# Performance work log

Measured on AMD Instinct MI355X. Metric: run time of the kernel, lower is better.

## Reference

```python
import jax, jax.numpy as jnp
import numpy as np


def _ln(x, w, b):
    m = jnp.mean(x, axis=-1, keepdims=True)
    v = jnp.var(x, axis=-1, keepdims=True)
    return (x - m) / jnp.sqrt(v + 1e-5) * w + b


def setup_inputs() -> dict:
    B, T, C = 4, 2048, 1024
    E_RWKV, E = 2, 3          # 2 RWKV experts + 1 transformer expert
    H = 4 * C                 # RWKV FFN hidden
    S = 0.02                  # init scale
    key = jax.random.key(0)
    ks = jax.random.split(key, 20)
    d = {}
    d["x"] = jax.random.normal(ks[0], (B, T, C), jnp.float32)
    d["v_first"] = jax.random.normal(ks[1], (B, T, C), jnp.float32)
    d["capital_shares"] = jax.random.uniform(ks[2], (E,), jnp.float32)
    # layer norms
    d["ln1_w"] = jnp.ones((C,), jnp.float32)
    d["ln1_b"] = jnp.zeros((C,), jnp.float32)
    d["ln2_w"] = jnp.ones((C,), jnp.float32)
    d["ln2_b"] = jnp.zeros((C,), jnp.float32)
    # simplified RWKV time-mix (gated linear attention stand-in)
    d["Wr"] = S * jax.random.normal(ks[3], (C, C), jnp.float32)
    d["Wv"] = S * jax.random.normal(ks[4], (C, C), jnp.float32)
    d["Wo"] = S * jax.random.normal(ks[5], (C, C), jnp.float32)
    d["Ws"] = S * jax.random.normal(ks[6], (C, C), jnp.float32)
    # RWKV FFN experts (squared-ReLU channel mix)
    d["K_rwkv"] = S * jax.random.normal(ks[7], (E_RWKV, C, H), jnp.float32)
    d["V_rwkv"] = S * jax.random.normal(ks[8], (E_RWKV, H, C), jnp.float32)
    d["conf_rwkv"] = S * jax.random.normal(ks[9], (E_RWKV, C), jnp.float32)
    # transformer expert (state-gated)
    d["W1"] = S * jax.random.normal(ks[10], (C, C), jnp.float32)
    d["W2"] = S * jax.random.normal(ks[11], (C, C), jnp.float32)
    d["W3"] = S * jax.random.normal(ks[12], (C, C), jnp.float32)
    d["conf_trans"] = S * jax.random.normal(ks[13], (C,), jnp.float32)
    # critic
    d["w_diff"] = S * jax.random.normal(ks[14], (C,), jnp.float32)
    d["W_aff"] = S * jax.random.normal(ks[15], (C, E), jnp.float32)
    # bridge (h -> rwkv_state reconstruction)
    d["W_bridge"] = S * jax.random.normal(ks[16], (C, C), jnp.float32)
    return d


def reference(x, v_first, capital_shares, ln1_w, ln1_b, ln2_w, ln2_b,
              Wr, Wv, Wo, Ws, K_rwkv, V_rwkv, conf_rwkv,
              W1, W2, W3, conf_trans, w_diff, W_aff, W_bridge):
    B, T, C = x.shape
    # attention (simplified time-mix): gated linear projection + state head
    xln = _ln(x, ln1_w, ln1_b)
    att_out = (jax.nn.sigmoid(xln @ Wr) * (xln @ Wv)) @ Wo
    rwkv_state = xln @ Ws
    x = x + att_out
    h = _ln(x, ln2_w, ln2_b)

    # per-expert confidences  (B, T, E)
    conf_r = jax.nn.sigmoid(jnp.einsum('btc,ec->bte', h, conf_rwkv))
    conf_t = jax.nn.sigmoid(h @ conf_trans)[..., None]
    confidences = jnp.concatenate([conf_r, conf_t], axis=-1)
    E = confidences.shape[-1]

    # critic + market routing: bids = conf * capital * difficulty + affinity subsidy
    difficulty = jax.nn.sigmoid(h @ w_diff)[..., None]          # (B, T, 1)
    affinity = h @ W_aff                                         # (B, T, E)
    bids = confidences * capital_shares * difficulty + affinity
    winners = jnp.argmax(bids, axis=-1)                          # (B, T) int

    flat_h = h.reshape(-1, C)                # (N, C)
    flat_state = rwkv_state.reshape(-1, C)   # (N, C)
    flat_w = winners.reshape(-1)             # (N,)
    flat_conf = confidences.reshape(-1, E)

    # straight-through confidence scale: conf / (stop_grad(conf) + eps)
    win_conf = jnp.take_along_axis(flat_conf, flat_w[:, None], axis=1)  # (N, 1)
    scale = win_conf / (jax.lax.stop_gradient(win_conf) + 1e-6)

    # expert compute (dense-per-expert, combined by winner mask -> same math
    # as gather/scatter dispatch in the torch loop)
    hr = jnp.square(jax.nn.relu(jnp.einsum('nc,ech->enh', flat_h, K_rwkv)))
    out_rwkv = jnp.einsum('enh,ehc->enc', hr, V_rwkv)            # (E_rwkv, N, C)
    out_trans = ((flat_h @ W1) * jax.nn.sigmoid(flat_state @ W2)) @ W3
    all_out = jnp.concatenate([out_rwkv, out_trans[None]], axis=0)  # (E, N, C)

    onehot = jax.nn.one_hot(flat_w, E, dtype=flat_h.dtype)       # (N, E)
    final = jnp.einsum('ne,enc->nc', onehot, all_out) * scale    # (N, C)
    return x + final.reshape(B, T, C)
```

## Files before the change

### kernel.cpp

```cpp
#include <hip/hip_runtime.h>
#include <stdint.h>


#define N_TOK 8192
#define C_DIM 1024
#define H_DIM 4096

typedef unsigned short u16;
typedef __attribute__((ext_vector_type(8))) short short8;
typedef _Float16 half8 __attribute__((ext_vector_type(8)));
typedef __attribute__((ext_vector_type(4))) float floatx4;

__device__ __forceinline__ float b2f(u16 u) {
  union { unsigned u; float f; } v; v.u = ((unsigned)u) << 16; return v.f;
}
__device__ __forceinline__ u16 f2b(float f) {
  union { float f; unsigned u; } v; v.f = f;
  unsigned r = v.u + 0x7fffu + ((v.u >> 16) & 1u);
  return (u16)(r >> 16);
}
__device__ __forceinline__ u16 f2h(float f) {
  union { _Float16 h; u16 u; } v; v.h = (_Float16)f; return v.u;
}
__device__ __forceinline__ float sigf(float x) { return 1.f / (1.f + __expf(-x)); }

typedef __attribute__((address_space(3))) unsigned int lds_uint;
typedef const __attribute__((address_space(1))) unsigned int glob_uint;
__device__ __forceinline__ void gld16(u16* lds, const u16* g) {
  __builtin_amdgcn_global_load_lds((glob_uint*)g, (lds_uint*)lds, 16, 0, 0);
}
__device__ __forceinline__ floatx4 mf(short8 a, short8 b, floatx4 c) {
  return __builtin_amdgcn_mfma_f32_16x16x32_bf16(a, b, c, 0, 0, 0);
}
__device__ __forceinline__ floatx4 mfh(half8 a, half8 b, floatx4 c) {
  return __builtin_amdgcn_mfma_f32_16x16x32_f16(a, b, c, 0, 0, 0);
}
__device__ __forceinline__ void stage2(u16* s, const u16* g, int K, int base,
                                       int c0, int c1, int k0) {
  gld16(s + c0 * 8, g + (size_t)(base + (c0 >> 2)) * K + k0 + (c0 & 3) * 8);
  gld16(s + c1 * 8, g + (size_t)(base + (c1 >> 2)) * K + k0 + (c1 & 3) * 8);
}
__device__ __forceinline__ void stage1(u16* s, const u16* g, int K, int base,
                                       int c, int k0) {
  gld16(s + c * 8, g + (size_t)(base + (c >> 2)) * K + k0 + (c & 3) * 8);
}
template <typename V>
__device__ __forceinline__ void fragN(V* f, const u16* s, int wo, int fr, int fk, int n) {
  for (int i = 0; i < n; i++) f[i] = *(const V*)(s + (wo + i * 16 + fr) * 32 + fk);
}

__global__ __launch_bounds__(256) void gemm_rv(
    const u16* __restrict__ Ahi, const u16* __restrict__ Alo,
    const u16* __restrict__ Brh, const u16* __restrict__ Brl,
    const u16* __restrict__ Bvh, const u16* __restrict__ Bvl,
    int K, int NC, u16* __restrict__ Ghi, u16* __restrict__ Glo,
    u16* __restrict__ G16) {
  __shared__ __align__(16) u16 sAh[4096], sAl[4096];
  __shared__ __align__(16) u16 sRh[2048], sRl[2048], sVh[2048], sVl[2048];
  const int tid = threadIdx.x, lane = tid & 63, wave = tid >> 6;
  const int rowbase = blockIdx.y * 128, colbase = blockIdx.x * 64;
  const int wm = (wave >> 1) * 64, wn = (wave & 1) * 32;
  floatx4 ar[4][2] = {}, av[4][2] = {};
  const int c0 = tid, c1 = tid + 256;
  for (int k0 = 0; k0 < K; k0 += 32) {
    __syncthreads();
    stage2(sAh, Ahi, K, rowbase, c0, c1, k0);
    stage2(sAl, Alo, K, rowbase, c0, c1, k0);
    stage1(sRh, Brh, K, colbase, c0, k0);
    stage1(sRl, Brl, K, colbase, c0, k0);
    stage1(sVh, Bvh, K, colbase, c0, k0);
    stage1(sVl, Bvl, K, colbase, c0, k0);
    __syncthreads();
    const int fr = lane & 15, fk = (lane >> 4) * 8;
    short8 ah[4], al[4], rh[2], rl[2], vh[2], vl[2];
    fragN(ah, sAh, wm, fr, fk, 4); fragN(al, sAl, wm, fr, fk, 4);
    fragN(rh, sRh, wn, fr, fk, 2); fragN(rl, sRl, wn, fr, fk, 2);
    fragN(vh, sVh, wn, fr, fk, 2); fragN(vl, sVl, wn, fr, fk, 2);
#pragma unroll
    for (int mi = 0; mi < 4; mi++)
#pragma unroll
      for (int ni = 0; ni < 2; ni++) {
        ar[mi][ni] = mf(ah[mi], rh[ni], ar[mi][ni]);
        ar[mi][ni] = mf(ah[mi], rl[ni], ar[mi][ni]);
        ar[mi][ni] = mf(al[mi], rh[ni], ar[mi][ni]);
        av[mi][ni] = mf(ah[mi], vh[ni], av[mi][ni]);
        av[mi][ni] = mf(ah[mi], vl[ni], av[mi][ni]);
        av[mi][ni] = mf(al[mi], vh[ni], av[mi][ni]);
      }
  }
  const int col0 = lane & 15, row0 = (lane >> 4) * 4;
#pragma unroll
  for (int mi = 0; mi < 4; mi++)
#pragma unroll
    for (int ni = 0; ni < 2; ni++)
#pragma unroll
      for (int r = 0; r < 4; r++) {
        const int row = rowbase + wm + mi * 16 + row0 + r;
        const int col = colbase + wn + ni * 16 + col0;
        const size_t idx = (size_t)row * NC + col;
        const float g = sigf(ar[mi][ni][r]) * av[mi][ni][r];
        const u16 h = f2b(g);
        Ghi[idx] = h;
        Glo[idx] = f2b(g - b2f(h));
        G16[idx] = f2h(g);
      }
}

__global__ __launch_bounds__(256) void gemm_wo_f16(
    const u16* __restrict__ A, const u16* __restrict__ BT, int K, int NC,
    const float* __restrict__ Xin, float* __restrict__ Xnew) {
  __shared__ __align__(16) u16 sA[4096], sB[2048];
  const int tid = threadIdx.x, lane = tid & 63, wave = tid >> 6;
  const int rowbase = blockIdx.y * 128, colbase = blockIdx.x * 64;
  const int wm = (wave >> 1) * 64, wn = (wave & 1) * 32;
  floatx4 acc[4][2] = {};
  const int c0 = tid, c1 = tid + 256;
  for (int k0 = 0; k0 < K; k0 += 32) {
    __syncthreads();
    stage2(sA, A, K, rowbase, c0, c1, k0);
    stage1(sB, BT, K, colbase, c0, k0);
    __syncthreads();
    const int fr = lane & 15, fk = (lane >> 4) * 8;
    half8 af[4], bf[2];
    fragN(af, sA, wm, fr, fk, 4);
    fragN(bf, sB, wn, fr, fk, 2);
#pragma unroll
    for (int mi = 0; mi < 4; mi++)
#pragma unroll
      for (int ni = 0; ni < 2; ni++)
        acc[mi][ni] = mfh(af[mi], bf[ni], acc[mi][ni]);
  }
  const int col0 = lane & 15, row0 = (lane >> 4) * 4;
#pragma unroll
  for (int mi = 0; mi < 4; mi++)
#pragma unroll
    for (int ni = 0; ni < 2; ni++)
#pragma unroll
      for (int r = 0; r < 4; r++) {
        const int row = rowbase + wm + mi * 16 + row0 + r;
        const int col = colbase + wn + ni * 16 + col0;
        const size_t idx = (size_t)row * NC + col;
        Xnew[idx] = Xin[idx] + acc[mi][ni][r];
      }
}

__global__ __launch_bounds__(256) void gemm_t12b(
    const u16* __restrict__ A1, const u16* __restrict__ A2,
    const int* __restrict__ idxA,
    const u16* __restrict__ B1, const u16* __restrict__ B2, int K, int NC,
    const int* __restrict__ cntp, u16* __restrict__ Cout) {
  const int cnt = *cntp;
  if ((int)blockIdx.y * 128 >= cnt) return;
  __shared__ __align__(16) u16 s1[4096], s2[4096], sB1[2048], sB2[2048];
  const int tid = threadIdx.x, lane = tid & 63, wave = tid >> 6;
  const int rowbase = blockIdx.y * 128, colbase = blockIdx.x * 64;
  const int wm = (wave >> 1) * 64, wn = (wave & 1) * 32;
  floatx4 a1[4][2] = {}, a2[4][2] = {};
  const int c0 = tid, c1 = tid + 256;
  const int g0 = idxA[rowbase + (c0 >> 2)], g1 = idxA[rowbase + (c1 >> 2)];
  const u16* p10 = A1 + (size_t)g0 * K + (c0 & 3) * 8;
  const u16* p11 = A1 + (size_t)g1 * K + (c1 & 3) * 8;
  const u16* p20 = A2 + (size_t)g0 * K + (c0 & 3) * 8;
  const u16* p21 = A2 + (size_t)g1 * K + (c1 & 3) * 8;
  for (int k0 = 0; k0 < K; k0 += 32) {
    __syncthreads();
    gld16(s1 + c0 * 8, p10 + k0);
    gld16(s1 + c1 * 8, p11 + k0);
    gld16(s2 + c0 * 8, p20 + k0);
    gld16(s2 + c1 * 8, p21 + k0);
    stage1(sB1, B1, K, colbase, c0, k0);
    stage1(sB2, B2, K, colbase, c0, k0);
    __syncthreads();
    const int fr = lane & 15, fk = (lane >> 4) * 8;
    short8 f1[4], f2[4], b1[2], b2[2];
    fragN(f1, s1, wm, fr, fk, 4); fragN(f2, s2, wm, fr, fk, 4);
    fragN(b1, sB1, wn, fr, fk, 2); fragN(b2, sB2, wn, fr, fk, 2);
#pragma unroll
    for (int mi = 0; mi < 4; mi++)
#pragma unroll
      for (int ni = 0; ni < 2; ni++) {
        a1[mi][ni] = mf(f1[mi], b1[ni], a1[mi][ni]);
        a2[mi][ni] = mf(f2[mi], b2[ni], a2[mi][ni]);
      }
  }
  const int col0 = lane & 15, row0 = (lane >> 4) * 4;
#pragma unroll
  for (int mi = 0; mi < 4; mi++)
#pragma unroll
    for (int ni = 0; ni < 2; ni++)
#pragma unroll
      for (int r = 0; r < 4; r++) {
        const int row = rowbase + wm + mi * 16 + row0 + r;
        const int col = colbase + wn + ni * 16 + col0;
        Cout[(size_t)row * NC + col] =
            f2b(a1[mi][ni][r] * sigf(a2[mi][ni][r]));
      }
}

__global__ __launch_bounds__(256) void tvgemm(
    const u16* __restrict__ A, const u16* __restrict__ BT,
    const int* __restrict__ cntp, const int* __restrict__ idxO,
    const float* __restrict__ x_new, const float* __restrict__ scalep,
    float* __restrict__ out) {
  const int cnt = *cntp;
  const int rowbase = blockIdx.y * 128;
  if (rowbase >= cnt) return;
  __shared__ __align__(16) u16 sA[4096], sB[2048];
  const int tid = threadIdx.x, lane = tid & 63, wave = tid >> 6;
  const int colbase = blockIdx.x * 64;
  const int wm = (wave >> 1) * 64, wn = (wave & 1) * 32;
  floatx4 acc[4][2] = {};
  const int c0 = tid, c1 = tid + 256;
  for (int k0 = 0; k0 < C_DIM; k0 += 32) {
    __syncthreads();
    stage2(sA, A, C_DIM, rowbase, c0, c1, k0);
    stage1(sB, BT, C_DIM, colbase, c0, k0);
    __syncthreads();
    const int fr = lane & 15, fk = (lane >> 4) * 8;
    short8 af[4], bf[2];
    fragN(af, sA, wm, fr, fk, 4);
    fragN(bf, sB, wn, fr, fk, 2);
#pragma unroll
    for (int mi = 0; mi < 4; mi++)
#pragma unroll
      for (int ni = 0; ni < 2; ni++)
        acc[mi][ni] = mf(af[mi], bf[ni], acc[mi][ni]);
  }
  const int col0 = lane & 15, row0 = (lane >> 4) * 4;
#pragma unroll
  for (int mi = 0; mi < 4; mi++)
#pragma unroll
    for (int ni = 0; ni < 2; ni++)
#pragma unroll
      for (int r = 0; r < 4; r++) {
        const int row = rowbase + wm + mi * 16 + row0 + r;
        if (row < cnt) {
          const int col = colbase + wn + ni * 16 + col0;
          const int g = idxO[row];
          const size_t o = (size_t)g * C_DIM + col;
          out[o] = x_new[o] + acc[mi][ni][r] * scalep[g];
        }
      }
}

__global__ __launch_bounds__(256) void kgemm2(
    const u16* __restrict__ A, const int* __restrict__ idx,
    const u16* __restrict__ KT0p, const u16* __restrict__ KT1p,
    const int* __restrict__ counts, int base,
    u16* __restrict__ hr0, u16* __restrict__ hr1) {
  const int e = blockIdx.z;
  const int cnt = counts[e] - base;
  const int rowbase = blockIdx.y * 128;
  if (rowbase >= cnt) return;
  const u16* BT = e ? KT1p : KT0p;
  const int* idxA = idx + e * N_TOK + base;
  u16* Cout = e ? hr1 : hr0;
  __shared__ __align__(16) u16 sA[4096], sB[4096];
  const int tid = threadIdx.x, lane = tid & 63, wave = tid >> 6;
  const int colbase = blockIdx.x * 128;
  const int wm = (wave >> 1) * 64, wn = (wave & 1) * 64;
  floatx4 acc[4][4] = {};
  const int c0 = tid, c1 = tid + 256;
  const int g0 = idxA[rowbase + (c0 >> 2)], g1 = idxA[rowbase + (c1 >> 2)];
  const u16* pA0 = A + (size_t)g0 * C_DIM + (c0 & 3) * 8;
  const u16* pA1 = A + (size_t)g1 * C_DIM + (c1 & 3) * 8;
  const u16* pB0 = BT + (size_t)(colbase + (c0 >> 2)) * C_DIM + (c0 & 3) * 8;
  const u16* pB1 = BT + (size_t)(colbase + (c1 >> 2)) * C_DIM + (c1 & 3) * 8;
  for (int k0 = 0; k0 < C_DIM; k0 += 32) {
    __syncthreads();
    gld16(sA + c0 * 8, pA0 + k0);
    gld16(sA + c1 * 8, pA1 + k0);
    gld16(sB + c0 * 8, pB0 + k0);
    gld16(sB + c1 * 8, pB1 + k0);
    __syncthreads();
    const int fr = lane & 15, fk = (lane >> 4) * 8;
    short8 af[4], bf[4];
    fragN(af, sA, wm, fr, fk, 4);
    fragN(bf, sB, wn, fr, fk, 4);
#pragma unroll
    for (int mi = 0; mi < 4; mi++)
#pragma unroll
      for (int ni = 0; ni < 4; ni++)
        acc[mi][ni] = mf(af[mi], bf[ni], acc[mi][ni]);
  }
  const int col0 = lane & 15, row00 = (lane >> 4) * 4;
#pragma unroll
  for (int mi = 0; mi < 4; mi++)
#pragma unroll
    for (int ni = 0; ni < 4; ni++)
#pragma unroll
      for (int r = 0; r < 4; r++) {
        const int row = rowbase + wm + mi * 16 + row00 + r;
        const int col = colbase + wn + ni * 16 + col0;
        const float v = acc[mi][ni][r];
        const float t = v > 0.f ? v * v : 0.f;
        Cout[(size_t)row * H_DIM + col] = f2b(t);
      }
}

__global__ __launch_bounds__(256) void vgemm_rwkv(
    const u16* __restrict__ hr0, const u16* __restrict__ hr1,
    const u16* __restrict__ VT0p, const u16* __restrict__ VT1p,
    const int* __restrict__ counts, int base,
    const int* __restrict__ idx, const float* __restrict__ x_new,
    const float* __restrict__ scalep, float* __restrict__ out) {
  const int e = blockIdx.z;
  const int cnt = counts[e] - base;
  const int rowbase = blockIdx.y * 128;
  if (rowbase >= cnt) return;
  const u16* A = e ? hr1 : hr0;
  const u16* BT = e ? VT1p : VT0p;
  const int* idxO = idx + e * N_TOK + base;
  __shared__ __align__(16) u16 sA[4096], sB[2048];
  const int tid = threadIdx.x, lane = tid & 63, wave = tid >> 6;
  const int colbase = blockIdx.x * 64;
  const int wm = (wave >> 1) * 64, wn = (wave & 1) * 32;
  floatx4 acc[4][2] = {};
  const int c0 = tid, c1 = tid + 256;
  for (int k0 = 0; k0 < H_DIM; k0 += 32) {
    __syncthreads();
    stage2(sA, A, H_DIM, rowbase, c0, c1, k0);
    stage1(sB, BT, H_DIM, colbase, c0, k0);
    __syncthreads();
    const int fr = lane & 15, fk = (lane >> 4) * 8;
    short8 af[4], bf[2];
    fragN(af, sA, wm, fr, fk, 4);
    fragN(bf, sB, wn, fr, fk, 2);
#pragma unroll
    for (int mi = 0; mi < 4; mi++)
#pragma unroll
      for (int ni = 0; ni < 2; ni++)
        acc[mi][ni] = mf(af[mi], bf[ni], acc[mi][ni]);
  }
  const int col0 = lane & 15, row0 = (lane >> 4) * 4;
#pragma unroll
  for (int mi = 0; mi < 4; mi++)
#pragma unroll
    for (int ni = 0; ni < 2; ni++)
#pragma unroll
      for (int r = 0; r < 4; r++) {
        const int row = rowbase + wm + mi * 16 + row0 + r;
        if (row < cnt) {
          const int col = colbase + wn + ni * 16 + col0;
          const int g = idxO[row];
          const size_t o = (size_t)g * C_DIM + col;
          out[o] = x_new[o] + acc[mi][ni][r] * scalep[g];
        }
      }
}

template <int EPI>
__global__ __launch_bounds__(256) void ggemm(
    const u16* __restrict__ A, const int* __restrict__ idxA,
    const u16* __restrict__ BT, int K, int NC,
    const int* __restrict__ cntp, int base,
    u16* __restrict__ Cout,
    const float* __restrict__ x_new, const float* __restrict__ scalep,
    const int* __restrict__ idxO, float* __restrict__ out) {
  const int cnt = cntp ? (*cntp - base) : (int)(gridDim.y * 128);
  if ((int)blockIdx.y * 128 >= cnt) return;
  __shared__ __align__(16) u16 sA[4096], sB[4096];
  const int tid = threadIdx.x, lane = tid & 63, wave = tid >> 6;
  const int rowbase = blockIdx.y * 128, colbase = blockIdx.x * 128;
  const int wm = (wave >> 1) * 64, wn = (wave & 1) * 64;
  floatx4 acc[4][4] = {};
  const int c0 = tid, c1 = tid + 256;
  const int r0 = rowbase + (c0 >> 2), r1 = rowbase + (c1 >> 2);
  const int g0 = idxA ? idxA[base + r0] : r0;
  const int g1 = idxA ? idxA[base + r1] : r1;
  const u16* pA0 = A + (size_t)g0 * K + (c0 & 3) * 8;
  const u16* pA1 = A + (size_t)g1 * K + (c1 & 3) * 8;
  const u16* pB0 = BT + (size_t)(colbase + (c0 >> 2)) * K + (c0 & 3) * 8;
  const u16* pB1 = BT + (size_t)(colbase + (c1 >> 2)) * K + (c1 & 3) * 8;
  for (int k0 = 0; k0 < K; k0 += 32) {
    __syncthreads();
    gld16(sA + c0 * 8, pA0 + k0);
    gld16(sA + c1 * 8, pA1 + k0);
    gld16(sB + c0 * 8, pB0 + k0);
    gld16(sB + c1 * 8, pB1 + k0);
    __syncthreads();
    const int fr = lane & 15, fk = (lane >> 4) * 8;
    short8 af[4], bf[4];
    fragN(af, sA, wm, fr, fk, 4);
    fragN(bf, sB, wn, fr, fk, 4);
#pragma unroll
    for (int mi = 0; mi < 4; mi++)
#pragma unroll
      for (int ni = 0; ni < 4; ni++)
        acc[mi][ni] = mf(af[mi], bf[ni], acc[mi][ni]);
  }
  const int col0 = lane & 15, row00 = (lane >> 4) * 4;
#pragma unroll
  for (int mi = 0; mi < 4; mi++)
#pragma unroll
    for (int ni = 0; ni < 4; ni++)
#pragma unroll
      for (int r = 0; r < 4; r++) {
        const int row = rowbase + wm + mi * 16 + row00 + r;
        const int col = colbase + wn + ni * 16 + col0;
        const float v = acc[mi][ni][r];
        if constexpr (EPI == 0) {
          Cout[(size_t)row * NC + col] = f2b(v);
        } else if constexpr (EPI == 2) {
          const float t = v > 0.f ? v * v : 0.f;
          Cout[(size_t)row * NC + col] = f2b(t);
        } else {
          if (row < cnt) {
            const int g = idxO[base + row];
            const size_t o = (size_t)g * NC + col;
            out[o] = x_new[o] + v * scalep[g];
          }
        }
      }
}

struct CCBatchArgs {
  const float *Wr, *Wv, *Wo, *W1, *W2, *W3;
  u16 *WrTh, *WrTl, *WvTh, *WvTl, *WoT16, *W1T, *W2T, *W3T;
};
__global__ __launch_bounds__(256) void transpose_cc_batch(CCBatchArgs a) {
  __shared__ float tile[32][33];
  const int z = blockIdx.z;
  const float* in; u16* oh; u16* ol = nullptr; int mode;
  switch (z) {
    case 0: in = a.Wr; oh = a.WrTh; ol = a.WrTl; mode = 1; break;
    case 1: in = a.Wv; oh = a.WvTh; ol = a.WvTl; mode = 1; break;
    case 2: in = a.Wo; oh = a.WoT16; mode = 2; break;
    case 3: in = a.W1; oh = a.W1T; mode = 0; break;
    case 4: in = a.W2; oh = a.W2T; mode = 0; break;
    default: in = a.W3; oh = a.W3T; mode = 0; break;
  }
  const int tx = threadIdx.x & 31, ty = threadIdx.x >> 5;
  const int bx = blockIdx.x * 32, by = blockIdx.y * 32;
#pragma unroll
  for (int i = 0; i < 32; i += 8)
    tile[ty + i][tx] = in[(size_t)(by + ty + i) * C_DIM + bx + tx];
  __syncthreads();
#pragma unroll
  for (int i = 0; i < 32; i += 8) {
    const float v = tile[tx][ty + i];
    const size_t o = (size_t)(bx + ty + i) * C_DIM + by + tx;
    if (mode == 2) {
      oh[o] = f2h(v);
    } else {
      const u16 h = f2b(v);
      oh[o] = h;
      if (mode == 1) ol[o] = f2b(v - b2f(h));
    }
  }
}

__global__ __launch_bounds__(256) void transpose_kv(
    const float* __restrict__ in, u16* __restrict__ o0, u16* __restrict__ o1,
    int R, int Cc) {
  __shared__ float tile[32][33];
  const float* ip = in + (size_t)blockIdx.z * R * Cc;
  u16* oh = blockIdx.z ? o1 : o0;
  const int tx = threadIdx.x & 31, ty = threadIdx.x >> 5;
  const int bx = blockIdx.x * 32, by = blockIdx.y * 32;
#pragma unroll
  for (int i = 0; i < 32; i += 8)
    tile[ty + i][tx] = ip[(size_t)(by + ty + i) * Cc + bx + tx];
  __syncthreads();
#pragma unroll
  for (int i = 0; i < 32; i += 8)
    oh[(size_t)(bx + ty + i) * R + by + tx] = f2b(tile[tx][ty + i]);
}

__global__ __launch_bounds__(256) void cast_kernel(const float* __restrict__ in,
                                                   u16* __restrict__ o, int n) {
  const int i = blockIdx.x * 256 + threadIdx.x;
  if (i < n) o[i] = f2b(in[i]);
}

__global__ __launch_bounds__(256) void ln_kernel(
    const float* __restrict__ x, const float* __restrict__ w,
    const float* __restrict__ b, u16* __restrict__ oh, u16* __restrict__ ol) {
  const int row = blockIdx.x, tid = threadIdx.x;
  const float* xr = x + (size_t)row * C_DIM;
  float vals[4], s = 0.f, ss = 0.f;
#pragma unroll
  for (int i = 0; i < 4; i++) {
    const float t = xr[tid + i * 256];
    vals[i] = t; s += t; ss += t * t;
  }
  for (int off = 32; off; off >>= 1) {
    s += __shfl_xor(s, off, 64);
    ss += __shfl_xor(ss, off, 64);
  }
  __shared__ float red[8];
  const int lane = tid & 63, wave = tid >> 6;
  if (lane == 0) { red[wave] = s; red[4 + wave] = ss; }
  __syncthreads();
  const float S = red[0] + red[1] + red[2] + red[3];
  const float SS = red[4] + red[5] + red[6] + red[7];
  const float mean = S * (1.f / C_DIM);
  const float var = SS * (1.f / C_DIM) - mean * mean;
  const float inv = rsqrtf(var + 1e-5f);
#pragma unroll
  for (int i = 0; i < 4; i++) {
    const int c = tid + i * 256;
    const float y = (vals[i] - mean) * inv * w[c] + b[c];
    const u16 h = f2b(y);
    oh[(size_t)row * C_DIM + c] = h;
    ol[(size_t)row * C_DIM + c] = f2b(y - b2f(h));
  }
}

__global__ __launch_bounds__(256) void prep_vec(
    const float* __restrict__ ln2w, const float* __restrict__ ln2b,
    const float* __restrict__ conf_rwkv, const float* __restrict__ conf_trans,
    const float* __restrict__ w_diff, const float* __restrict__ W_aff,
    float* __restrict__ p, float* __restrict__ sg, float* __restrict__ sb) {
  const int j = blockIdx.x, tid = threadIdx.x;
  float gs = 0.f, bs = 0.f;
#pragma unroll
  for (int i = 0; i < 4; i++) {
    const int c = tid + i * 256;
    float wv;
    if (j == 0) wv = conf_rwkv[c];
    else if (j == 1) wv = conf_rwkv[C_DIM + c];
    else if (j == 2) wv = conf_trans[c];
    else if (j == 3) wv = w_diff[c];
    else wv = W_aff[c * 3 + (j - 4)];
    const float pv = ln2w[c] * wv;
    p[j * C_DIM + c] = pv;
    gs += pv;
    bs += ln2b[c] * wv;
  }
  for (int off = 32; off; off >>= 1) {
    gs += __shfl_xor(gs, off, 64);
    bs += __shfl_xor(bs, off, 64);
  }
  __shared__ float red[8];
  const int lane = tid & 63, wave = tid >> 6;
  if (lane == 0) { red[wave] = gs; red[4 + wave] = bs; }
  __syncthreads();
  if (tid == 0) {
    sg[j] = red[0] + red[1] + red[2] + red[3];
    sb[j] = red[4] + red[5] + red[6] + red[7];
  }
}

__global__ __launch_bounds__(256) void ugemv(
    const float* __restrict__ Wo, const float* __restrict__ p,
    float* __restrict__ u) {
  const int o = blockIdx.x * 4 + (threadIdx.x >> 6);
  const int lane = threadIdx.x & 63;
  const int j = o >> 10, k = o & 1023;
  float s = 0.f;
#pragma unroll
  for (int i = 0; i < 16; i++) {
    const int c = lane + i * 64;
    s += Wo[(size_t)k * C_DIM + c] * p[j * C_DIM + c];
  }
  for (int off = 32; off; off >>= 1) s += __shfl_xor(s, off, 64);
  if (lane == 0) u[o] = s;
}

__global__ __launch_bounds__(256) void route_kernel(
    const float* __restrict__ x, const float* __restrict__ xn,
    const u16* __restrict__ ghi, const u16* __restrict__ glo,
    const float* __restrict__ p, const float* __restrict__ u,
    const float* __restrict__ sg, const float* __restrict__ sb,
    const float* __restrict__ ln2w, const float* __restrict__ ln2b,
    const float* __restrict__ capital,
    int* __restrict__ winner, float* __restrict__ scale, u16* __restrict__ oh,
    int* __restrict__ pz, int nz) {
  {
    const int i = blockIdx.x * 256 + threadIdx.x;
    if (i < nz) pz[i] = 0;
  }
  const int token = blockIdx.x * 4 + (threadIdx.x >> 6);
  const int lane = threadIdx.x & 63;
  const float* xnr = xn + (size_t)token * C_DIM;
  float xv[16], s = 0.f, ss = 0.f;
#pragma unroll
  for (int i = 0; i < 16; i++) {
    const float t = xnr[lane + i * 64];
    xv[i] = t; s += t; ss += t * t;
  }
  for (int off = 32; off; off >>= 1) {
    s += __shfl_xor(s, off, 64);
    ss += __shfl_xor(ss, off, 64);
  }
  const float mean = s * (1.f / C_DIM);
  const float var = ss * (1.f / C_DIM) - mean * mean;
  const float inv = rsqrtf(var + 1e-5f);
  float acc[7] = {};
#pragma unroll
  for (int i = 0; i < 16; i++) {
    const int c = lane + i * 64;
    oh[(size_t)token * C_DIM + c] = f2b((xv[i] - mean) * inv * ln2w[c] + ln2b[c]);
    const float xc = x[(size_t)token * C_DIM + c];
    const float gc = b2f(ghi[(size_t)token * C_DIM + c]) +
                     b2f(glo[(size_t)token * C_DIM + c]);
#pragma unroll
    for (int j = 0; j < 7; j++)
      acc[j] += xc * p[j * C_DIM + c] + gc * u[j * C_DIM + c];
  }
  for (int off = 32; off; off >>= 1)
#pragma unroll
    for (int j = 0; j < 7; j++) acc[j] += __shfl_xor(acc[j], off, 64);
  if (lane == 0) {
    float hw[7];
#pragma unroll
    for (int j = 0; j < 7; j++) hw[j] = acc[j] * inv - mean * inv * sg[j] + sb[j];
    const float conf[3] = {1.f / (1.f + expf(-hw[0])), 1.f / (1.f + expf(-hw[1])),
                           1.f / (1.f + expf(-hw[2]))};
    const float diff = 1.f / (1.f + expf(-hw[3]));
    int best = 0; float bb = -1e30f;
#pragma unroll
    for (int e = 0; e < 3; e++) {
      const float bid = conf[e] * capital[e] * diff + hw[4 + e];
      if (bid > bb) { bb = bid; best = e; }
    }
    winner[token] = best;
    scale[token] = conf[best] / (conf[best] + 1e-6f);
  }
}

__global__ __launch_bounds__(256) void compact_kernel(
    const int* __restrict__ winner, int* __restrict__ idx, int* __restrict__ counts) {
  const int t = blockIdx.x * 256 + threadIdx.x;
  const int w = winner[t];
  const int pos = atomicAdd(counts + w, 1);
  idx[w * N_TOK + pos] = t;
}

extern "C" void kernel_launch(void* const* d_in, const int* in_sizes, int n_in,
                              void* d_out, int out_size, void* d_ws, size_t ws_size,
                              hipStream_t stream) {
  const float* x = (const float*)d_in[0];
  const float* capital = (const float*)d_in[2];
  const float* ln1w = (const float*)d_in[3];
  const float* ln1b = (const float*)d_in[4];
  const float* ln2w = (const float*)d_in[5];
  const float* ln2b = (const float*)d_in[6];
  const float* Wr = (const float*)d_in[7];
  const float* Wv = (const float*)d_in[8];
  const float* Wo = (const float*)d_in[9];
  const float* Wsm = (const float*)d_in[10];
  const float* Krwkv = (const float*)d_in[11];
  const float* Vrwkv = (const float*)d_in[12];
  const float* conf_rwkv = (const float*)d_in[13];
  const float* W1 = (const float*)d_in[14];
  const float* W2 = (const float*)d_in[15];
  const float* W3 = (const float*)d_in[16];
  const float* conf_trans = (const float*)d_in[17];
  const float* w_diff = (const float*)d_in[18];
  const float* W_aff = (const float*)d_in[19];
  float* out = (float*)d_out;

  char* ws = (char*)d_ws;
  size_t off = 0;
  auto alloc = [&](size_t bytes) -> char* {
    char* pp = ws + off;
    off += (bytes + 255) & ~(size_t)255;
    return pp;
  };
  const size_t CC = (size_t)C_DIM * C_DIM * 2;
  const size_t CH = (size_t)C_DIM * H_DIM * 2;
  const size_t NCb = (size_t)N_TOK * C_DIM * 2;
  u16* WrTh = (u16*)alloc(CC); u16* WrTl = (u16*)alloc(CC);
  u16* WvTh = (u16*)alloc(CC); u16* WvTl = (u16*)alloc(CC);
  u16* WoT16 = (u16*)alloc(CC);
  u16* W1T = (u16*)alloc(CC);
  u16* W2T = (u16*)alloc(CC);
  u16* W3T = (u16*)alloc(CC);
  u16* Wsb = (u16*)alloc(CC);
  u16* MT  = (u16*)alloc(CC);
  u16* KT0 = (u16*)alloc(CH);
  u16* VT0 = (u16*)alloc(CH);
  u16* KT1 = (u16*)alloc(CH);
  u16* VT1 = (u16*)alloc(CH);
  u16* xlnh = (u16*)alloc(NCb);
  u16* xlnl = (u16*)alloc(NCb);
  u16* ghi = (u16*)alloc(NCb);
  u16* glo = (u16*)alloc(NCb);
  u16* g16 = (u16*)alloc(NCb);
  float* x_new = (float*)alloc((size_t)N_TOK * C_DIM * 4);
  u16* hr1 = (u16*)alloc((size_t)4096 * H_DIM * 2);
  u16* hr0 = glo;
  int* idx = (int*)alloc(3 * N_TOK * 4);
  int* counts = (int*)alloc(256);
  int* winner = (int*)alloc(N_TOK * 4);
  float* scalep = (float*)alloc(N_TOK * 4);
  float* pvec = (float*)alloc(7 * C_DIM * 4);
  float* uvec = (float*)alloc(7 * C_DIM * 4);
  float* sgv = (float*)alloc(256);
  float* sbv = (float*)alloc(256);

  const dim3 blk(256);
  CCBatchArgs ta = {Wr, Wv, Wo, W1, W2, W3,
                    WrTh, WrTl, WvTh, WvTl, WoT16, W1T, W2T, W3T};
  transpose_cc_batch<<<dim3(32, 32, 6), blk, 0, stream>>>(ta);
  transpose_kv<<<dim3(H_DIM / 32, C_DIM / 32, 2), blk, 0, stream>>>(
      Krwkv, KT0, KT1, C_DIM, H_DIM);
  transpose_kv<<<dim3(C_DIM / 32, H_DIM / 32, 2), blk, 0, stream>>>(
      Vrwkv, VT0, VT1, H_DIM, C_DIM);
  cast_kernel<<<(C_DIM * C_DIM) / 256, blk, 0, stream>>>(Wsm, Wsb, C_DIM * C_DIM);
  ggemm<0><<<dim3(8, 8), blk, 0, stream>>>(W2T, nullptr, Wsb, C_DIM, C_DIM,
      nullptr, 0, MT, nullptr, nullptr, nullptr, nullptr);
  prep_vec<<<7, blk, 0, stream>>>(ln2w, ln2b, conf_rwkv, conf_trans, w_diff,
                                  W_aff, pvec, sgv, sbv);
  ugemv<<<7 * C_DIM / 4, blk, 0, stream>>>(Wo, pvec, uvec);

  ln_kernel<<<N_TOK, blk, 0, stream>>>(x, ln1w, ln1b, xlnh, xlnl);

  gemm_rv<<<dim3(C_DIM / 64, N_TOK / 128), blk, 0, stream>>>(
      xlnh, xlnl, WrTh, WrTl, WvTh, WvTl, C_DIM, C_DIM, ghi, glo, g16);
  gemm_wo_f16<<<dim3(C_DIM / 64, N_TOK / 128), blk, 0, stream>>>(
      g16, WoT16, C_DIM, C_DIM, x, x_new);
  u16* hb = xlnl;
  route_kernel<<<N_TOK / 4, blk, 0, stream>>>(x, x_new, ghi, glo, pvec, uvec,
      sgv, sbv, ln2w, ln2b, capital, winner, scalep, hb, idx, 3 * N_TOK + 64);
  compact_kernel<<<N_TOK / 256, blk, 0, stream>>>(winner, idx, counts);

  int* idx2 = idx + 2 * N_TOK;
  u16* tg = ghi;
  gemm_t12b<<<dim3(C_DIM / 64, N_TOK / 128), blk, 0, stream>>>(
      hb, xlnh, idx2, W1T, MT, C_DIM, C_DIM, counts + 2, tg);
  tvgemm<<<dim3(C_DIM / 64, N_TOK / 128), blk, 0, stream>>>(
      tg, W3T, counts + 2, idx2, x_new, scalep, out);

  for (int c = 0; c < 2; c++) {
    const int base = c * 4096;
    kgemm2<<<dim3(H_DIM / 128, 32, 2), blk, 0, stream>>>(
        hb, idx, KT0, KT1, counts, base, hr0, hr1);
    vgemm_rwkv<<<dim3(C_DIM / 64, 32, 2), blk, 0, stream>>>(
        hr0, hr1, VT0, VT1, counts, base, idx, x_new, scalep, out);
  }
}
```

Before: 778.0 us.

## Merge transformer expert GEMMs into RWKV expert launches and double K-step

After: 721.1 us. 1.08x faster.

```diff
diff --git a/kernel.cpp b/kernel.cpp
--- a/kernel.cpp
+++ b/kernel.cpp
@@ -109,21 +109,30 @@
 __global__ __launch_bounds__(256) void gemm_wo_f16(
     const u16* __restrict__ A, const u16* __restrict__ BT, int K, int NC,
     const float* __restrict__ Xin, float* __restrict__ Xnew) {
-  __shared__ __align__(16) u16 sA[4096], sB[2048];
+  __shared__ __align__(16) u16 sA0[4096], sA1[4096], sB0[2048], sB1[2048];
   const int tid = threadIdx.x, lane = tid & 63, wave = tid >> 6;
   const int rowbase = blockIdx.y * 128, colbase = blockIdx.x * 64;
   const int wm = (wave >> 1) * 64, wn = (wave & 1) * 32;
   floatx4 acc[4][2] = {};
   const int c0 = tid, c1 = tid + 256;
-  for (int k0 = 0; k0 < K; k0 += 32) {
+  for (int k0 = 0; k0 < K; k0 += 64) {
     __syncthreads();
-    stage2(sA, A, K, rowbase, c0, c1, k0);
-    stage1(sB, BT, K, colbase, c0, k0);
+    stage2(sA0, A, K, rowbase, c0, c1, k0);
+    stage2(sA1, A, K, rowbase, c0, c1, k0 + 32);
+    stage1(sB0, BT, K, colbase, c0, k0);
+    stage1(sB1, BT, K, colbase, c0, k0 + 32);
     __syncthreads();
     const int fr = lane & 15, fk = (lane >> 4) * 8;
     half8 af[4], bf[2];
-    fragN(af, sA, wm, fr, fk, 4);
-    fragN(bf, sB, wn, fr, fk, 2);
+    fragN(af, sA0, wm, fr, fk, 4);
+    fragN(bf, sB0, wn, fr, fk, 2);
+#pragma unroll
+    for (int mi = 0; mi < 4; mi++)
+#pragma unroll
+      for (int ni = 0; ni < 2; ni++)
+        acc[mi][ni] = mfh(af[mi], bf[ni], acc[mi][ni]);
+    fragN(af, sA1, wm, fr, fk, 4);
+    fragN(bf, sB1, wn, fr, fk, 2);
 #pragma unroll
     for (int mi = 0; mi < 4; mi++)
 #pragma unroll
@@ -144,188 +153,156 @@
       }
 }
 
-__global__ __launch_bounds__(256) void gemm_t12b(
-    const u16* __restrict__ A1, const u16* __restrict__ A2,
-    const int* __restrict__ idxA,
-    const u16* __restrict__ B1, const u16* __restrict__ B2, int K, int NC,
-    const int* __restrict__ cntp, u16* __restrict__ Cout) {
-  const int cnt = *cntp;
-  if ((int)blockIdx.y * 128 >= cnt) return;
-  __shared__ __align__(16) u16 s1[4096], s2[4096], sB1[2048], sB2[2048];
+__global__ __launch_bounds__(256) void expert_mid(
+    const u16* __restrict__ hb, const u16* __restrict__ xlnh,
+    const int* __restrict__ idx,
+    const u16* __restrict__ KT0p, const u16* __restrict__ KT1p,
+    const u16* __restrict__ W1T, const u16* __restrict__ MTp,
+    const int* __restrict__ counts, int base,
+    u16* __restrict__ hr0, u16* __restrict__ hr1, u16* __restrict__ tg) {
+  __shared__ __align__(16) u16 smem[12288];
+  const int z = blockIdx.z;
   const int tid = threadIdx.x, lane = tid & 63, wave = tid >> 6;
-  const int rowbase = blockIdx.y * 128, colbase = blockIdx.x * 64;
-  const int wm = (wave >> 1) * 64, wn = (wave & 1) * 32;
-  floatx4 a1[4][2] = {}, a2[4][2] = {};
+  const int rowbase = blockIdx.y * 128;
   const int c0 = tid, c1 = tid + 256;
-  const int g0 = idxA[rowbase + (c0 >> 2)], g1 = idxA[rowbase + (c1 >> 2)];
-  const u16* p10 = A1 + (size_t)g0 * K + (c0 & 3) * 8;
-  const u16* p11 = A1 + (size_t)g1 * K + (c1 & 3) * 8;
-  const u16* p20 = A2 + (size_t)g0 * K + (c0 & 3) * 8;
-  const u16* p21 = A2 + (size_t)g1 * K + (c1 & 3) * 8;
-  for (int k0 = 0; k0 < K; k0 += 32) {
-    __syncthreads();
-    gld16(s1 + c0 * 8, p10 + k0);
-    gld16(s1 + c1 * 8, p11 + k0);
-    gld16(s2 + c0 * 8, p20 + k0);
-    gld16(s2 + c1 * 8, p21 + k0);
-    stage1(sB1, B1, K, colbase, c0, k0);
-    stage1(sB2, B2, K, colbase, c0, k0);
-    __syncthreads();
-    const int fr = lane & 15, fk = (lane >> 4) * 8;
-    short8 f1[4], f2[4], b1[2], b2[2];
-    fragN(f1, s1, wm, fr, fk, 4); fragN(f2, s2, wm, fr, fk, 4);
-    fragN(b1, sB1, wn, fr, fk, 2); fragN(b2, sB2, wn, fr, fk, 2);
+  const int fr = lane & 15, fk = (lane >> 4) * 8;
+  const int col0 = lane & 15, row00 = (lane >> 4) * 4;
+  if (z < 2) {
+    const int cnt = counts[z] - base;
+    if (rowbase >= cnt) return;
+    const u16* BT = z ? KT1p : KT0p;
+    const int* idxA = idx + z * N_TOK + base;
+    u16* Cout = z ? hr1 : hr0;
+    u16* sA = smem;
+    u16* sB = smem + 4096;
+    const int colbase = blockIdx.x * 128;
+    const int wm = (wave >> 1) * 64, wn = (wave & 1) * 64;
+    floatx4 acc[4][4] = {};
+    const int g0 = idxA[rowbase + (c0 >> 2)], g1 = idxA[rowbase + (c1 >> 2)];
+    const u16* pA0 = hb + (size_t)g0 * C_DIM + (c0 & 3) * 8;
+    const u16* pA1 = hb + (size_t)g1 * C_DIM + (c1 & 3) * 8;
+    const u16* pB0 = BT + (size_t)(colbase + (c0 >> 2)) * C_DIM + (c0 & 3) * 8;
+    const u16* pB1 = BT + (size_t)(colbase + (c1 >> 2)) * C_DIM + (c1 & 3) * 8;
+    for (int k0 = 0; k0 < C_DIM; k0 += 32) {
+      __syncthreads();
+      gld16(sA + c0 * 8, pA0 + k0);
+      gld16(sA + c1 * 8, pA1 + k0);
+      gld16(sB + c0 * 8, pB0 + k0);
+      gld16(sB + c1 * 8, pB1 + k0);
+      __syncthreads();
+      short8 af[4], bf[4];
+      fragN(af, sA, wm, fr, fk, 4);
+      fragN(bf, sB, wn, fr, fk, 4);
+#pragma unroll
+      for (int mi = 0; mi < 4; mi++)
+#pragma unroll
+        for (int ni = 0; ni < 4; ni++)
+          acc[mi][ni] = mf(af[mi], bf[ni], acc[mi][ni]);
+    }
 #pragma unroll
     for (int mi = 0; mi < 4; mi++)
 #pragma unroll
-      for (int ni = 0; ni < 2; ni++) {
-        a1[mi][ni] = mf(f1[mi], b1[ni], a1[mi][ni]);
-        a2[mi][ni] = mf(f2[mi], b2[ni], a2[mi][ni]);
-      }
-  }
-  const int col0 = lane & 15, row0 = (lane >> 4) * 4;
-#pragma unroll
-  for (int mi = 0; mi < 4; mi++)
-#pragma unroll
-    for (int ni = 0; ni < 2; ni++)
-#pragma unroll
-      for (int r = 0; r < 4; r++) {
-        const int row = rowbase + wm + mi * 16 + row0 + r;
-        const int col = colbase + wn + ni * 16 + col0;
-        Cout[(size_t)row * NC + col] =
-            f2b(a1[mi][ni][r] * sigf(a2[mi][ni][r]));
-      }
-}
-
-__global__ __launch_bounds__(256) void tvgemm(
-    const u16* __restrict__ A, const u16* __restrict__ BT,
-    const int* __restrict__ cntp, const int* __restrict__ idxO,
+      for (int ni = 0; ni < 4; ni++)
+#pragma unroll
+        for (int r = 0; r < 4; r++) {
+          const int row = rowbase + wm + mi * 16 + row00 + r;
+          const int col = colbase + wn + ni * 16 + col0;
+          const float v = acc[mi][ni][r];
+          const float t = v > 0.f ? v * v : 0.f;
+          Cout[(size_t)row * H_DIM + col] = f2b(t);
+        }
+  } else {
+    if (blockIdx.x >= 16) return;
+    const int cnt = counts[2] - base;
+    if (rowbase >= cnt) return;
+    const int* idxA = idx + 2 * N_TOK + base;
+    u16* s1 = smem;
+    u16* s2 = smem + 4096;
+    u16* sB1 = smem + 8192;
+    u16* sB2 = smem + 10240;
+    const int colbase = blockIdx.x * 64;
+    const int wm = (wave >> 1) * 64, wn = (wave & 1) * 32;
+    floatx4 a1[4][2] = {}, a2[4][2] = {};
+    const int g0 = idxA[rowbase + (c0 >> 2)], g1 = idxA[rowbase + (c1 >> 2)];
+    const u16* p10 = hb + (size_t)g0 * C_DIM + (c0 & 3) * 8;
+    const u16* p11 = hb + (size_t)g1 * C_DIM + (c1 & 3) * 8;
+    const u16* p20 = xlnh + (size_t)g0 * C_DIM + (c0 & 3) * 8;
+    const u16* p21 = xlnh + (size_t)g1 * C_DIM + (c1 & 3) * 8;
+    for (int k0 = 0; k0 < C_DIM; k0 += 32) {
+      __syncthreads();
+      gld16(s1 + c0 * 8, p10 + k0);
+      gld16(s1 + c1 * 8, p11 + k0);
+      gld16(s2 + c0 * 8, p20 + k0);
+      gld16(s2 + c1 * 8, p21 + k0);
+      stage1(sB1, W1T, C_DIM, colbase, c0, k0);
+      stage1(sB2, MTp, C_DIM, colbase, c0, k0);
+      __syncthreads();
+      short8 f1[4], f2[4], b1[2], b2[2];
+      fragN(f1, s1, wm, fr, fk, 4); fragN(f2, s2, wm, fr, fk, 4);
+      fragN(b1, sB1, wn, fr, fk, 2); fragN(b2, sB2, wn, fr, fk, 2);
+#pragma unroll
+      for (int mi = 0; mi < 4; mi++)
+#pragma unroll
+        for (int ni = 0; ni < 2; ni++) {
+          a1[mi][ni] = mf(f1[mi], b1[ni], a1[mi][ni]);
+          a2[mi][ni] = mf(f2[mi], b2[ni], a2[mi][ni]);
+        }
+    }
+#pragma unroll
+    for (int mi = 0; mi < 4; mi++)
+#pragma unroll
+      for (int ni = 0; ni < 2; ni++)
+#pragma unroll
+        for (int r = 0; r < 4; r++) {
+          const int row = rowbase + wm + mi * 16 + row00 + r;
+          const int col = colbase + wn + ni * 16 + col0;
+          tg[(size_t)(base + row) * C_DIM + col] =
+              f2b(a1[mi][ni][r] * sigf(a2[mi][ni][r]));
+        }
+  }
+}
+
+__global__ __launch_bounds__(256) void vgemm3(
+    const u16* __restrict__ hr0, const u16* __restrict__ hr1,
+    const u16* __restrict__ tg,
+    const u16* __restrict__ VT0p, const u16* __restrict__ VT1p,
+    const u16* __restrict__ W3T,
+    const int* __restrict__ counts, int base, const int* __restrict__ idx,
     const float* __restrict__ x_new, const float* __restrict__ scalep,
     float* __restrict__ out) {
-  const int cnt = *cntp;
+  const int z = blockIdx.z;
+  const int cnt = counts[z] - base;
   const int rowbase = blockIdx.y * 128;
   if (rowbase >= cnt) return;
-  __shared__ __align__(16) u16 sA[4096], sB[2048];
+  const u16* A; const u16* BT; int K; int arow;
+  if (z == 0)      { A = hr0; BT = VT0p; K = H_DIM; arow = rowbase; }
+  else if (z == 1) { A = hr1; BT = VT1p; K = H_DIM; arow = rowbase; }
+  else             { A = tg;  BT = W3T;  K = C_DIM; arow = base + rowbase; }
+  const int* idxO = idx + z * N_TOK + base;
+  __shared__ __align__(16) u16 sA0[4096], sA1[4096], sB0[2048], sB1[2048];
   const int tid = threadIdx.x, lane = tid & 63, wave = tid >> 6;
   const int colbase = blockIdx.x * 64;
   const int wm = (wave >> 1) * 64, wn = (wave & 1) * 32;
   floatx4 acc[4][2] = {};
   const int c0 = tid, c1 = tid + 256;
-  for (int k0 = 0; k0 < C_DIM; k0 += 32) {
+  for (int k0 = 0; k0 < K; k0 += 64) {
     __syncthreads();
-    stage2(sA, A, C_DIM, rowbase, c0, c1, k0);
-    stage1(sB, BT, C_DIM, colbase, c0, k0);
+    stage2(sA0, A, K, arow, c0, c1, k0);
+    stage2(sA1, A, K, arow, c0, c1, k0 + 32);
+    stage1(sB0, BT, K, colbase, c0, k0);
+    stage1(sB1, BT, K, colbase, c0, k0 + 32);
     __syncthreads();
     const int fr = lane & 15, fk = (lane >> 4) * 8;
     short8 af[4], bf[2];
-    fragN(af, sA, wm, fr, fk, 4);
-    fragN(bf, sB, wn, fr, fk, 2);
+    fragN(af, sA0, wm, fr, fk, 4);
+    fragN(bf, sB0, wn, fr, fk, 2);
 #pragma unroll
     for (int mi = 0; mi < 4; mi++)
 #pragma unroll
       for (int ni = 0; ni < 2; ni++)
         acc[mi][ni] = mf(af[mi], bf[ni], acc[mi][ni]);
-  }
-  const int col0 = lane & 15, row0 = (lane >> 4) * 4;
-#pragma unroll
-  for (int mi = 0; mi < 4; mi++)
-#pragma unroll
-    for (int ni = 0; ni < 2; ni++)
-#pragma unroll
-      for (int r = 0; r < 4; r++) {
-        const int row = rowbase + wm + mi * 16 + row0 + r;
-        if (row < cnt) {
-          const int col = colbase + wn + ni * 16 + col0;
-          const int g = idxO[row];
-          const size_t o = (size_t)g * C_DIM + col;
-          out[o] = x_new[o] + acc[mi][ni][r] * scalep[g];
-        }
-      }
-}
-
-__global__ __launch_bounds__(256) void kgemm2(
-    const u16* __restrict__ A, const int* __restrict__ idx,
-    const u16* __restrict__ KT0p, const u16* __restrict__ KT1p,
-    const int* __restrict__ counts, int base,
-    u16* __restrict__ hr0, u16* __restrict__ hr1) {
-  const int e = blockIdx.z;
-  const int cnt = counts[e] - base;
-  const int rowbase = blockIdx.y * 128;
-  if (rowbase >= cnt) return;
-  const u16* BT = e ? KT1p : KT0p;
-  const int* idxA = idx + e * N_TOK + base;
-  u16* Cout = e ? hr1 : hr0;
-  __shared__ __align__(16) u16 sA[4096], sB[4096];
-  const int tid = threadIdx.x, lane = tid & 63, wave = tid >> 6;
-  const int colbase = blockIdx.x * 128;
-  const int wm = (wave >> 1) * 64, wn = (wave & 1) * 64;
-  floatx4 acc[4][4] = {};
-  const int c0 = tid, c1 = tid + 256;
-  const int g0 = idxA[rowbase + (c0 >> 2)], g1 = idxA[rowbase + (c1 >> 2)];
-  const u16* pA0 = A + (size_t)g0 * C_DIM + (c0 & 3) * 8;
-  const u16* pA1 = A + (size_t)g1 * C_DIM + (c1 & 3) * 8;
-  const u16* pB0 = BT + (size_t)(colbase + (c0 >> 2)) * C_DIM + (c0 & 3) * 8;
-  const u16* pB1 = BT + (size_t)(colbase + (c1 >> 2)) * C_DIM + (c1 & 3) * 8;
-  for (int k0 = 0; k0 < C_DIM; k0 += 32) {
-    __syncthreads();
-    gld16(sA + c0 * 8, pA0 + k0);
-    gld16(sA + c1 * 8, pA1 + k0);
-    gld16(sB + c0 * 8, pB0 + k0);
-    gld16(sB + c1 * 8, pB1 + k0);
-    __syncthreads();
-    const int fr = lane & 15, fk = (lane >> 4) * 8;
-    short8 af[4], bf[4];
-    fragN(af, sA, wm, fr, fk, 4);
-    fragN(bf, sB, wn, fr, fk, 4);
-#pragma unroll
-    for (int mi = 0; mi < 4; mi++)
-#pragma unroll
-      for (int ni = 0; ni < 4; ni++)
-        acc[mi][ni] = mf(af[mi], bf[ni], acc[mi][ni]);
-  }
-  const int col0 = lane & 15, row00 = (lane >> 4) * 4;
-#pragma unroll
-  for (int mi = 0; mi < 4; mi++)
-#pragma unroll
-    for (int ni = 0; ni < 4; ni++)
-#pragma unroll
-      for (int r = 0; r < 4; r++) {
-        const int row = rowbase + wm + mi * 16 + row00 + r;
-        const int col = colbase + wn + ni * 16 + col0;
-        const float v = acc[mi][ni][r];
-        const float t = v > 0.f ? v * v : 0.f;
-        Cout[(size_t)row * H_DIM + col] = f2b(t);
-      }
-}
-
-__global__ __launch_bounds__(256) void vgemm_rwkv(
-    const u16* __restrict__ hr0, const u16* __restrict__ hr1,
-    const u16* __restrict__ VT0p, const u16* __restrict__ VT1p,
-    const int* __restrict__ counts, int base,
-    const int* __restrict__ idx, const float* __restrict__ x_new,
-    const float* __restrict__ scalep, float* __restrict__ out) {
-  const int e = blockIdx.z;
-  const int cnt = counts[e] - base;
-  const int rowbase = blockIdx.y * 128;
-  if (rowbase >= cnt) return;
-  const u16* A = e ? hr1 : hr0;
-  const u16* BT = e ? VT1p : VT0p;
-  const int* idxO = idx + e * N_TOK + base;
-  __shared__ __align__(16) u16 sA[4096], sB[2048];
-  const int tid = threadIdx.x, lane = tid & 63, wave = tid >> 6;
-  const int colbase = blockIdx.x * 64;
-  const int wm = (wave >> 1) * 64, wn = (wave & 1) * 32;
-  floatx4 acc[4][2] = {};
-  const int c0 = tid, c1 = tid + 256;
-  for (int k0 = 0; k0 < H_DIM; k0 += 32) {
-    __syncthreads();
-    stage2(sA, A, H_DIM, rowbase, c0, c1, k0);
-    stage1(sB, BT, H_DIM, colbase, c0, k0);
-    __syncthreads();
-    const int fr = lane & 15, fk = (lane >> 4) * 8;
-    short8 af[4], bf[2];
-    fragN(af, sA, wm, fr, fk, 4);
-    fragN(bf, sB, wn, fr, fk, 2);
+    fragN(af, sA1, wm, fr, fk, 4);
+    fragN(bf, sB1, wn, fr, fk, 2);
 #pragma unroll
     for (int mi = 0; mi < 4; mi++)
 #pragma unroll
@@ -717,18 +694,12 @@
       sgv, sbv, ln2w, ln2b, capital, winner, scalep, hb, idx, 3 * N_TOK + 64);
   compact_kernel<<<N_TOK / 256, blk, 0, stream>>>(winner, idx, counts);
 
-  int* idx2 = idx + 2 * N_TOK;
   u16* tg = ghi;
-  gemm_t12b<<<dim3(C_DIM / 64, N_TOK / 128), blk, 0, stream>>>(
-      hb, xlnh, idx2, W1T, MT, C_DIM, C_DIM, counts + 2, tg);
-  tvgemm<<<dim3(C_DIM / 64, N_TOK / 128), blk, 0, stream>>>(
-      tg, W3T, counts + 2, idx2, x_new, scalep, out);
-
   for (int c = 0; c < 2; c++) {
     const int base = c * 4096;
-    kgemm2<<<dim3(H_DIM / 128, 32, 2), blk, 0, stream>>>(
-        hb, idx, KT0, KT1, counts, base, hr0, hr1);
-    vgemm_rwkv<<<dim3(C_DIM / 64, 32, 2), blk, 0, stream>>>(
-        hr0, hr1, VT0, VT1, counts, base, idx, x_new, scalep, out);
-  }
-}
+    expert_mid<<<dim3(H_DIM / 128, 32, 3), blk, 0, stream>>>(
+        hb, xlnh, idx, KT0, KT1, W1T, MT, counts, base, hr0, hr1, tg);
+    vgemm3<<<dim3(C_DIM / 64, 32, 3), blk, 0, stream>>>(
+        hr0, hr1, tg, VT0, VT1, W3T, counts, base, idx, x_new, scalep, out);
+  }
+}
```
